# Kernel optimization log

Measured on AMD Instinct MI355X. Metric: run time of the kernel, lower is better.

## Reference

```python
import jax, jax.numpy as jnp
import numpy as np

EPS = 1e-8

def setup_inputs() -> dict:
    key = jax.random.key(0)
    k1, k2, k3 = jax.random.split(key, 3)
    B, N, L = 4096, 8192, 256
    logits = jax.random.normal(k1, (B, N), dtype=jnp.float32)
    positive_ids = jax.random.randint(k2, (B, L), 0, N, dtype=jnp.int64)
    positive_weights = jax.random.uniform(k3, (B, L), dtype=jnp.float32)
    return {"logits": logits, "positive_ids": positive_ids, "positive_weights": positive_weights}

def reference(logits, positive_ids, positive_weights):
    # gather positive logits: [B, L]
    gathered = jnp.take_along_axis(logits, positive_ids, axis=1)
    w = positive_weights.astype(jnp.float32)
    w = w / jnp.maximum(w.sum(axis=-1, keepdims=True), EPS)
    # sort by weight descending
    order = jnp.argsort(-w, axis=-1)
    ordered_logits = jnp.take_along_axis(gathered, order, axis=1)
    ordered_weights = jnp.take_along_axis(w, order, axis=1)
    # suffix logsumexp in one reverse cumulative pass: [B, L]
    suffix_lse = jax.lax.cumlogsumexp(ordered_logits, axis=1, reverse=True)
    listmle = jnp.sum(ordered_weights * (suffix_lse - ordered_logits), axis=-1)
    return jnp.mean(listmle)
```

## Files before the change

### kernel.cpp

```cpp
#include <hip/hip_runtime.h>
#include <hip/hip_bf16.h>
#include <math.h>

#define BROWS 4096
#define NCOLS 8192
#define LLEN  256
#define EPSV  1e-8f

__global__ void zero_out_kernel(float* out) { out[0] = 0.0f; }

__global__ __launch_bounds__(256) void listmle_kernel(
    const float* __restrict__ logits,
    const int*   __restrict__ ids,
    const float* __restrict__ weights,
    float*       __restrict__ out)
{
    __shared__ float s_g[LLEN];
    __shared__ unsigned long long s_key[LLEN];
    __shared__ float s_m[LLEN];
    __shared__ float s_s[LLEN];
    __shared__ float s_red[4];

    const int tid = threadIdx.x;
    const int b   = blockIdx.x;

    float w  = weights[(size_t)b * LLEN + tid];
    int   id = ids[(size_t)b * LLEN + tid];
    float g  = logits[(size_t)b * NCOLS + id];

    s_g[tid] = g;
    s_key[tid] = ((unsigned long long)__float_as_uint(w) << 32)
               | (unsigned)(LLEN - 1 - tid);

    float v = w;
    #pragma unroll
    for (int o = 32; o > 0; o >>= 1) v += __shfl_down(v, o);
    if ((tid & 63) == 0) s_red[tid >> 6] = v;
    __syncthreads();
    float wsum = s_red[0] + s_red[1] + s_red[2] + s_red[3];

    for (int k = 2; k <= LLEN; k <<= 1) {
        for (int j = k >> 1; j > 0; j >>= 1) {
            int ixj = tid ^ j;
            if (ixj > tid) {
                unsigned long long a = s_key[tid];
                unsigned long long c = s_key[ixj];
                bool up = ((tid & k) == 0);
                if ((a < c) == up) { s_key[tid] = c; s_key[ixj] = a; }
            }
            __syncthreads();
        }
    }

    unsigned long long key = s_key[tid];
    float ow  = __uint_as_float((unsigned)(key >> 32));
    int   pos = (LLEN - 1) - (int)(key & 0xFFFFFFFFull);
    float og  = s_g[pos];

    float m = og, ssum = 1.0f;
    s_m[tid] = m; s_s[tid] = ssum;
    __syncthreads();
    #pragma unroll
    for (int off = 1; off < LLEN; off <<= 1) {
        float mp = 0.0f, sp = 0.0f;
        bool has = (tid + off) < LLEN;
        if (has) { mp = s_m[tid + off]; sp = s_s[tid + off]; }
        __syncthreads();
        if (has) {
            float nm = fmaxf(m, mp);
            ssum = ssum * expf(m - nm) + sp * expf(mp - nm);
            m = nm;
            s_m[tid] = m; s_s[tid] = ssum;
        }
        __syncthreads();
    }
    float suffix_lse = m + logf(ssum);

    float t = ow * (suffix_lse - og);
    #pragma unroll
    for (int o = 32; o > 0; o >>= 1) t += __shfl_down(t, o);
    if ((tid & 63) == 0) s_red[tid >> 6] = t;
    __syncthreads();

    if (tid == 0) {
        float tot  = s_red[0] + s_red[1] + s_red[2] + s_red[3];
        float loss = tot / fmaxf(wsum, EPSV);
        atomicAdd(out, loss * (1.0f / (float)BROWS));
    }
}

extern "C" void kernel_launch(void* const* d_in, const int* in_sizes, int n_in,
                              void* d_out, int out_size, void* d_ws, size_t ws_size,
                              hipStream_t stream) {
    const float* logits  = (const float*)d_in[0];
    const int*   ids     = (const int*)d_in[1];
    const float* weights = (const float*)d_in[2];
    float* out = (float*)d_out;

    zero_out_kernel<<<dim3(1), dim3(1), 0, stream>>>(out);
    listmle_kernel<<<dim3(BROWS), dim3(LLEN), 0, stream>>>(logits, ids, weights, out);
}
```

Before: 221.7 us.

## Use wavefront shuffles for bitonic sort and suffix logsumexp scan

The bitonic sort now keeps each key in registers and exchanges partners with __shfl_xor for strides under 64, using double-buffered shared memory and a single barrier only for cross-wave strides. The suffix logsumexp scan becomes an in-wavefront shuffle scan followed by combining the per-wave aggregates, replacing the 16 block barriers of the shared-memory scan. The weight-sum reduction is folded into the final reduction, and fast __expf replaces expf. This removes most __syncthreads and LDS traffic, at the cost of slightly lower exp precision.

After: 220.7 us. Within noise of the previous version (-0.5%).

```diff
diff --git a/kernel.cpp b/kernel.cpp
--- a/kernel.cpp
+++ b/kernel.cpp
@@ -16,74 +16,86 @@
     float*       __restrict__ out)
 {
     __shared__ float s_g[LLEN];
-    __shared__ unsigned long long s_key[LLEN];
-    __shared__ float s_m[LLEN];
-    __shared__ float s_s[LLEN];
-    __shared__ float s_red[4];
+    __shared__ unsigned long long s_key[2][LLEN];
+    __shared__ float s_aggm[4], s_aggs[4];
+    __shared__ float s_redt[4], s_redw[4];
 
-    const int tid = threadIdx.x;
-    const int b   = blockIdx.x;
+    const int tid  = threadIdx.x;
+    const int lane = tid & 63;
+    const int wv   = tid >> 6;
+    const int b    = blockIdx.x;
 
     float w  = weights[(size_t)b * LLEN + tid];
     int   id = ids[(size_t)b * LLEN + tid];
     float g  = logits[(size_t)b * NCOLS + id];
+    s_g[tid] = g;
 
-    s_g[tid] = g;
-    s_key[tid] = ((unsigned long long)__float_as_uint(w) << 32)
-               | (unsigned)(LLEN - 1 - tid);
+    unsigned key_hi = __float_as_uint(w);
+    unsigned key_lo = (unsigned)(LLEN - 1 - tid);
 
-    float v = w;
+    int phase = 0;
     #pragma unroll
-    for (int o = 32; o > 0; o >>= 1) v += __shfl_down(v, o);
-    if ((tid & 63) == 0) s_red[tid >> 6] = v;
-    __syncthreads();
-    float wsum = s_red[0] + s_red[1] + s_red[2] + s_red[3];
-
     for (int k = 2; k <= LLEN; k <<= 1) {
+        #pragma unroll
         for (int j = k >> 1; j > 0; j >>= 1) {
-            int ixj = tid ^ j;
-            if (ixj > tid) {
-                unsigned long long a = s_key[tid];
-                unsigned long long c = s_key[ixj];
-                bool up = ((tid & k) == 0);
-                if ((a < c) == up) { s_key[tid] = c; s_key[ixj] = a; }
+            const bool keep_max = (((tid & k) == 0) == ((tid & j) == 0));
+            unsigned p_hi, p_lo;
+            if (j < 64) {
+                p_hi = __shfl_xor(key_hi, j);
+                p_lo = __shfl_xor(key_lo, j);
+            } else {
+                s_key[phase][tid] = ((unsigned long long)key_hi << 32) | key_lo;
+                __syncthreads();
+                unsigned long long p = s_key[phase][tid ^ j];
+                p_hi = (unsigned)(p >> 32);
+                p_lo = (unsigned)p;
+                phase ^= 1;
             }
-            __syncthreads();
+            const bool pgt  = (p_hi > key_hi) || (p_hi == key_hi && p_lo > key_lo);
+            if (pgt == keep_max) { key_hi = p_hi; key_lo = p_lo; }
         }
     }
 
-    unsigned long long key = s_key[tid];
-    float ow  = __uint_as_float((unsigned)(key >> 32));
-    int   pos = (LLEN - 1) - (int)(key & 0xFFFFFFFFull);
+    float ow  = __uint_as_float(key_hi);
+    int   pos = (LLEN - 1) - (int)key_lo;
     float og  = s_g[pos];
 
-    float m = og, ssum = 1.0f;
-    s_m[tid] = m; s_s[tid] = ssum;
+    float m = og, s = 1.0f;
+    #pragma unroll
+    for (int off = 1; off < 64; off <<= 1) {
+        float mp = __shfl_down(m, off);
+        float sp = __shfl_down(s, off);
+        if (lane + off < 64) {
+            float nm = fmaxf(m, mp);
+            s = s * __expf(m - nm) + sp * __expf(mp - nm);
+            m = nm;
+        }
+    }
+    if (lane == 0) { s_aggm[wv] = m; s_aggs[wv] = s; }
     __syncthreads();
     #pragma unroll
-    for (int off = 1; off < LLEN; off <<= 1) {
-        float mp = 0.0f, sp = 0.0f;
-        bool has = (tid + off) < LLEN;
-        if (has) { mp = s_m[tid + off]; sp = s_s[tid + off]; }
-        __syncthreads();
-        if (has) {
+    for (int w2 = 0; w2 < 4; ++w2) {
+        if (w2 > wv) {
+            float mp = s_aggm[w2], sp = s_aggs[w2];
             float nm = fmaxf(m, mp);
-            ssum = ssum * expf(m - nm) + sp * expf(mp - nm);
+            s = s * __expf(m - nm) + sp * __expf(mp - nm);
             m = nm;
-            s_m[tid] = m; s_s[tid] = ssum;
         }
-        __syncthreads();
     }
-    float suffix_lse = m + logf(ssum);
+    float suffix_lse = m + logf(s);
 
-    float t = ow * (suffix_lse - og);
+    float t  = ow * (suffix_lse - og);
+    float ws = ow;
     #pragma unroll
-    for (int o = 32; o > 0; o >>= 1) t += __shfl_down(t, o);
-    if ((tid & 63) == 0) s_red[tid >> 6] = t;
+    for (int o = 32; o > 0; o >>= 1) {
+        t  += __shfl_down(t, o);
+        ws += __shfl_down(ws, o);
+    }
+    if (lane == 0) { s_redt[wv] = t; s_redw[wv] = ws; }
     __syncthreads();
-
     if (tid == 0) {
-        float tot  = s_red[0] + s_red[1] + s_red[2] + s_red[3];
+        float tot  = s_redt[0] + s_redt[1] + s_redt[2] + s_redt[3];
+        float wsum = s_redw[0] + s_redw[1] + s_redw[2] + s_redw[3];
         float loss = tot / fmaxf(wsum, EPSV);
         atomicAdd(out, loss * (1.0f / (float)BROWS));
     }
```
